# Kernel optimization log

Hardware: AMD Instinct MI355X
Metric: run time of the kernel (lower is better)

## Reference

```python
import jax, jax.numpy as jnp
import numpy as np

B, K, C, H, W = 8, 8, 128, 64, 64
RATE = 0.5
HW = H * W
NUM = int(RATE * HW)


def _l2norm(x, axis):
    # F.normalize: x / max(||x||, eps)
    n = jnp.linalg.norm(x, axis=axis, keepdims=True)
    return x / jnp.maximum(n, 1e-12)


def setup_inputs() -> dict:
    key = jax.random.key(0)
    k1, k2, k3 = jax.random.split(key, 3)
    feat = jax.random.normal(k1, (B, C, H, W), jnp.float32)
    refs = jax.random.normal(k2, (B, K, C, H, W), jnp.float32)
    sim = jax.random.uniform(k3, (B, K), jnp.float32)
    sim = sim / jnp.sum(sim, axis=1, keepdims=True)  # row-normalized as in Generator
    rng = np.random.default_rng(0)
    # random.sample -> unique spatial indices per batch row
    feat_indices = jnp.asarray(
        np.stack([rng.permutation(HW)[:NUM] for _ in range(B)]), jnp.int32)
    return {"feat": feat, "refs": refs, "similarity": sim,
            "feat_indices": feat_indices, "index": 0}


def reference(feat, refs, similarity, feat_indices, index):
    b, k, c, h, w = refs.shape
    hw = h * w
    n = k - 1
    # drop the base reference at `index`
    refs_ex = jnp.concatenate([refs[:, :index], refs[:, index + 1:]], axis=1)  # [b,n,c,h,w]
    base_sim = similarity[:, index]                                            # [b]
    ref_sims = jnp.concatenate([similarity[:, :index], similarity[:, index + 1:]], axis=1)  # [b,n]

    feat2 = feat.reshape(b, c, hw)                       # [b,c,hw]
    w_feat = _l2norm(jnp.swapaxes(feat2, 1, 2), 2)       # [b,hw,c], unit over c
    refs2 = refs_ex.reshape(b, n, c, hw)                 # [b,n,c,hw]
    w_refs = _l2norm(refs2, 2)                           # unit over c

    # gather the sampled query positions
    feat_select = jnp.take_along_axis(feat2, feat_indices[:, None, :], axis=2)   # [b,c,num]
    w_feat_sel = jnp.take_along_axis(w_feat, feat_indices[:, :, None], axis=1)   # [b,num,c]
    w_feat_sel = _l2norm(w_feat_sel, 2)

    def retrieve(args):
        w_ref, ref = args                                  # [b,c,hw] each
        fx = jnp.einsum('bqc,bch->bqh', w_feat_sel, w_ref)  # cosine scores [b,num,hw]
        idx = jnp.argmax(fx, axis=2)                        # top-1 -> [b,num]
        sel = jnp.take_along_axis(ref, idx[:, None, :], axis=2)  # [b,c,num]
        return idx, sel

    # sequential over n=k-1 refs (matches original loop, keeps peak memory at one
    # [b,num,hw] score matrix at a time)
    ref_idx, ref_sel = jax.lax.map(
        retrieve, (jnp.moveaxis(w_refs, 1, 0), jnp.moveaxis(refs2, 1, 0)))
    ref_indices = jnp.swapaxes(ref_idx, 0, 1)            # [b,n,num]
    ref_selects = jnp.moveaxis(ref_sel, 0, 1)            # [b,n,c,num]

    # similarity-weighted fusion
    fused = base_sim[:, None, None] * feat_select \
        + jnp.einsum('bn,bncq->bcq', ref_sims, ref_selects)   # [b,c,num]

    # batched scatter back into the feature map
    out = feat2.at[jnp.arange(b)[:, None, None],
                   jnp.arange(c)[None, :, None],
                   feat_indices[:, None, :]].set(fused)
    return out.reshape(b, c, h, w), feat_indices, ref_indices
```

## Files before the change

kernel.cpp:

```cpp
#include <hip/hip_runtime.h>
#include <math.h>

#define B_    8
#define K_    8
#define C_    128
#define HW_   4096
#define NUM_  2048
#define N_    7

#define WS_A_OFF    0
#define WS_SELQ_OFF (B_*NUM_*C_)
#define WS_KBUF_OFF (WS_SELQ_OFF + B_*K_*HW_)
#define WS_IDX_OFF  (WS_KBUF_OFF + B_*N_*NUM_*8)
#define WS_A2_OFF   (WS_IDX_OFF + B_*N_*NUM_)
#define WS_GHI_OFF  (WS_A2_OFF + B_*NUM_*C_)
#define GPLANE_V4   (B_*K_*16*HW_)

typedef __bf16 bf16x8 __attribute__((ext_vector_type(8)));
typedef float  f32x4  __attribute__((ext_vector_type(4)));
typedef unsigned int u32x4 __attribute__((ext_vector_type(4)));

static __device__ __forceinline__ f32x4 mf16(bf16x8 a, bf16x8 b, f32x4 c) {
    return __builtin_amdgcn_mfma_f32_16x16x32_bf16(a, b, c, 0, 0, 0);
}

static __device__ __forceinline__ unsigned bfhi16(float x) {
    unsigned b = __float_as_uint(x);
    return (b + 0x7fffu + ((b >> 16) & 1u)) >> 16;
}
static __device__ __forceinline__ void split2(float x, float y,
                                              unsigned &hp, unsigned &lp) {
    unsigned hx = bfhi16(x), hy = bfhi16(y);
    float rx = x - __uint_as_float(hx << 16);
    float ry = y - __uint_as_float(hy << 16);
    hp = hx | (hy << 16);
    lp = bfhi16(rx) | (bfhi16(ry) << 16);
}

static __device__ __forceinline__ float fmul_nc(float a, float b) {
    float r = a * b;
    asm volatile("" : "+v"(r));
    return r;
}
static __device__ __forceinline__ float fadd_nc(float a, float b) {
    float r = a + b;
    asm volatile("" : "+v"(r));
    return r;
}

static __device__ __forceinline__ void gll16(const u32x4* g, u32x4* l) {
    __builtin_amdgcn_global_load_lds(
        (const __attribute__((address_space(1))) void*)g,
        (__attribute__((address_space(3))) void*)l, 16, 0, 0);
}

__global__ void prep_split(const float* __restrict__ refs,
                           u32x4* __restrict__ Ghi,
                           u32x4* __restrict__ Glo) {
    __shared__ float part[8][32];
    __shared__ float ivs[32];
    int blk = blockIdx.x;
    int h0  = (blk & (HW_ / 32 - 1)) * 32;
    int bk  = blk >> 7;
    int t = threadIdx.x;
    int h = t & 31, oct = t >> 5;
    const float* p = refs + ((size_t)bk * C_ + oct * 16) * HW_ + h0 + h;
    float v[16];
    float ss = 0.f;
#pragma unroll
    for (int m = 0; m < 16; ++m) {
        v[m] = p[(size_t)m * HW_];
        ss = fmaf(v[m], v[m], ss);
    }
    part[oct][h] = ss;
    __syncthreads();
    if (t < 32) {
        float s = part[0][t];
#pragma unroll
        for (int o = 1; o < 8; ++o) s += part[o][t];
        ivs[t] = 1.0f / fmaxf(sqrtf(s), 1e-12f);
    }
    __syncthreads();
    float iv = ivs[h];
    u32x4 H0, L0, H1, L1;
#pragma unroll
    for (int m = 0; m < 4; ++m) {
        unsigned hp, lp;
        split2(v[2*m] * iv, v[2*m+1] * iv, hp, lp);
        H0[m] = hp; L0[m] = lp;
    }
#pragma unroll
    for (int m = 0; m < 4; ++m) {
        unsigned hp, lp;
        split2(v[8+2*m] * iv, v[9+2*m] * iv, hp, lp);
        H1[m] = hp; L1[m] = lp;
    }
    size_t o0 = (size_t)(bk * 16 + 2*oct)     * HW_ + h0 + h;
    size_t o1 = (size_t)(bk * 16 + 2*oct + 1) * HW_ + h0 + h;
    Ghi[o0] = H0; Glo[o0] = L0;
    Ghi[o1] = H1; Glo[o1] = L1;
}

__global__ void aprep2_kernel(const float* __restrict__ feat,
                              const int* __restrict__ fidx,
                              float* __restrict__ A,
                              float* __restrict__ A2,
                              int* __restrict__ selq,
                              float* __restrict__ out1) {
    int w    = (blockIdx.x * blockDim.x + threadIdx.x) >> 6;
    int lane = threadIdx.x & 63;
    int fi = fidx[w];
    int b  = w >> 11;
    const float* src = feat + (size_t)b * C_ * HW_ + fi;
    float v0 = src[(size_t)lane * HW_];
    float v1 = src[(size_t)(lane + 64) * HW_];
    float ss = fmaf(v0, v0, v1 * v1);
#pragma unroll
    for (int off = 32; off; off >>= 1) ss += __shfl_xor(ss, off);
    float rn = 1.0f / fmaxf(sqrtf(ss), 1e-12f);
    size_t o = (size_t)w * C_;
    A[o + lane]       = v0;
    A[o + lane + 64]  = v1;
    A2[o + lane]      = v0 * rn;
    A2[o + lane + 64] = v1 * rn;
    if (lane == 0) {
        selq[b * HW_ + fi] = w & (NUM_ - 1);
        out1[w] = (float)fi;
    }
}

__global__ __launch_bounds__(256, 4) void gemm_gll_topk2(
        const float* __restrict__ A2,
        const u32x4* __restrict__ Ghi, const u32x4* __restrict__ Glo,
        const int* __restrict__ pindex,
        uint4* __restrict__ kbuf) {
    __shared__ u32x4 Bsh[2][2][512];

    const int tid = threadIdx.x;
    const int l = tid & 63, wq = tid >> 6;
    const int ll = l & 15, lh = l >> 4;

    int bid = blockIdx.x;
    int swz = (bid & 7) * 224 + (bid >> 3);
    int pair = swz >> 5;
    int rem  = swz & 31;
    int qt = rem >> 1, hs = rem & 1;
    int b = pair / N_, n = pair % N_;
    int index = pindex[0];
    int ks = n + (n >= index ? 1 : 0);
    const int hbase0 = hs * 2048;

    const float* Ap = A2 + ((size_t)b * NUM_ + qt * 128 + wq * 32) * C_;
    const u32x4* Gh = Ghi + (size_t)(b * K_ + ks) * 16 * HW_ + hbase0;
    const u32x4* Gl = Glo + (size_t)(b * K_ + ks) * 16 * HW_ + hbase0;

    bf16x8 ahi[2][4], alo[2][4];
#pragma unroll
    for (int mf = 0; mf < 2; ++mf)
#pragma unroll
        for (int kk = 0; kk < 4; ++kk) {
            const float* ap = Ap + (mf * 16 + ll) * C_ + kk * 32 + lh * 8;
            float4 xa = *(const float4*)ap;
            float4 xb = *(const float4*)(ap + 4);
            float xs[8] = {xa.x, xa.y, xa.z, xa.w, xb.x, xb.y, xb.z, xb.w};
            u32x4 H, L;
#pragma unroll
            for (int p = 0; p < 4; ++p) {
                unsigned hp, lp;
                split2(xs[2*p], xs[2*p+1], hp, lp);
                H[p] = hp; L[p] = lp;
            }
            ahi[mf][kk] = __builtin_bit_cast(bf16x8, H);
            alo[mf][kk] = __builtin_bit_cast(bf16x8, L);
        }

    unsigned k1[8], k2[8];
#pragma unroll
    for (int rw = 0; rw < 8; ++rw) { k1[rw] = 0u; k2[rw] = 0u; }

    const int lin0 = tid, lin1 = 256 + tid;
    const size_t go0 = (size_t)(lin0 >> 5) * HW_ + (lin0 & 31);
    const size_t go1 = (size_t)(lin1 >> 5) * HW_ + (lin1 & 31);

#define STAGE(buf, htv) do {                                   \
        gll16(Gh + go0 + (htv), &Bsh[buf][0][lin0]);           \
        gll16(Gh + go1 + (htv), &Bsh[buf][0][lin1]);           \
        gll16(Gl + go0 + (htv), &Bsh[buf][1][lin0]);           \
        gll16(Gl + go1 + (htv), &Bsh[buf][1][lin1]);           \
    } while (0)

    STAGE(0, 0);
    __syncthreads();

    for (int t = 0; t < 64; ++t) {
        const int cur = t & 1;
        const int ht = t * 32;

        if (t < 63) STAGE(cur ^ 1, ht + 32);

        f32x4 acc[2][2];
#pragma unroll
        for (int mf = 0; mf < 2; ++mf)
#pragma unroll
            for (int nf = 0; nf < 2; ++nf) acc[mf][nf] = 6.0f;

#pragma unroll
        for (int kk = 0; kk < 4; ++kk) {
#pragma unroll
            for (int nf = 0; nf < 2; ++nf) {
                int off = (kk * 4 + lh) * 32 + nf * 16 + ll;
                bf16x8 bh = __builtin_bit_cast(bf16x8, Bsh[cur][0][off]);
                bf16x8 bl = __builtin_bit_cast(bf16x8, Bsh[cur][1][off]);
#pragma unroll
                for (int mf = 0; mf < 2; ++mf) {
                    f32x4 a_ = acc[mf][nf];
                    a_ = mf16(ahi[mf][kk], bh, a_);
                    a_ = mf16(ahi[mf][kk], bl, a_);
                    a_ = mf16(alo[mf][kk], bh, a_);
                    acc[mf][nf] = a_;
                }
            }
        }

#pragma unroll
        for (int nf = 0; nf < 2; ++nf) {
            unsigned hv = (unsigned)(hbase0 + ht + nf * 16 + ll);
#pragma unroll
            for (int mf = 0; mf < 2; ++mf)
#pragma unroll
                for (int r = 0; r < 4; ++r) {
                    int rw = mf * 4 + r;
                    unsigned u = __float_as_uint(acc[mf][nf][r]);
                    unsigned key = ((u & 0x007FFFF8u) << 9) | hv;
                    unsigned mn = min(k1[rw], key);
                    k1[rw] = max(k1[rw], key);
                    k2[rw] = max(k2[rw], mn);
                }
        }

        __syncthreads();
    }
#undef STAGE

#define CEU(X,Y) { if (mv[Y] > mv[X]) { unsigned t_ = mv[X]; mv[X] = mv[Y]; mv[Y] = t_; } }
#pragma unroll
    for (int rw = 0; rw < 8; ++rw) {
        unsigned av[4] = {k1[rw], k2[rw], 0u, 0u};
#pragma unroll
        for (int s = 1; s <= 8; s <<= 1) {
            unsigned bv[4];
#pragma unroll
            for (int j = 0; j < 4; ++j)
                bv[j] = (unsigned)__shfl_xor((int)av[j], s);
            unsigned mv[4];
#pragma unroll
            for (int j = 0; j < 4; ++j)
                mv[j] = (av[j] > bv[3-j]) ? av[j] : bv[3-j];
            CEU(0, 2) CEU(1, 3) CEU(0, 1) CEU(2, 3)
#pragma unroll
            for (int j = 0; j < 4; ++j) av[j] = mv[j];
        }
        if (ll == 0) {
            int q = qt * 128 + wq * 32 + (rw >> 2) * 16 + lh * 4 + (rw & 3);
            size_t o = ((size_t)(b * N_ + n) * NUM_ + q) * 2 + hs;
            kbuf[o] = make_uint4(av[0], av[1], av[2], av[3]);
        }
    }
#undef CEU
}

static __device__ float pairwise128_sumsq_div(const float* __restrict__ x,
                                              float d) {
    float r[8];
#pragma unroll
    for (int j = 0; j < 8; ++j) {
        float v = __fdiv_rn(x[j], d);
        r[j] = fmul_nc(v, v);
    }
    for (int i = 8; i < C_; i += 8) {
#pragma unroll
        for (int j = 0; j < 8; ++j) {
            float v = __fdiv_rn(x[i + j], d);
            r[j] = fadd_nc(r[j], fmul_nc(v, v));
        }
    }
    return fadd_nc(fadd_nc(fadd_nc(r[0], r[1]), fadd_nc(r[2], r[3])),
                   fadd_nc(fadd_nc(r[4], r[5]), fadd_nc(r[6], r[7])));
}

static __device__ float emul_score_batched(const float* __restrict__ w2a,
                                           const float* __restrict__ Rb,
                                           int h) {
    float rv[C_];
#pragma unroll
    for (int c = 0; c < C_; ++c) rv[c] = Rb[(size_t)c * HW_ + h];
    float sr = fmul_nc(rv[0], rv[0]);
#pragma unroll
    for (int c = 1; c < C_; ++c)
        sr = fadd_nc(sr, fmul_nc(rv[c], rv[c]));
    float nr = fmaxf(__fsqrt_rn(sr), 1e-12f);
    float acc = 0.f;
#pragma unroll
    for (int c = 0; c < C_; ++c) {
        float wr = __fdiv_rn(rv[c], nr);
        acc = fadd_nc(acc, fmul_nc(w2a[c], wr));
    }
    return acc;
}

__global__ __launch_bounds__(256, 1) void rescore_emul8(
        const float* __restrict__ A,
        const float* __restrict__ refs,
        const int* __restrict__ pindex,
        const uint4* __restrict__ kbuf,
        float thr,
        int* __restrict__ idxout,
        float* __restrict__ out2) {
    int r = blockIdx.x * blockDim.x + threadIdx.x;
    if (r >= B_ * N_ * NUM_) return;
    uint4 ka = kbuf[(size_t)r * 2 + 0];
    uint4 kb = kbuf[(size_t)r * 2 + 1];
    unsigned kk[8] = {ka.x, ka.y, ka.z, ka.w, kb.x, kb.y, kb.z, kb.w};
    unsigned s1 = 0u, s2 = 0u;
#pragma unroll
    for (int j = 0; j < 8; ++j) {
        unsigned mn = min(s1, kk[j]);
        s1 = max(s1, kk[j]);
        s2 = max(s2, mn);
    }
    int win;
    unsigned top = s1 >> 12;
    if ((float)(top - (s2 >> 12)) > thr) {
        win = (int)(s1 & 0xFFFu);
    } else {
        int q  = r & (NUM_ - 1);
        int bn = r >> 11;
        int b = bn / N_, n = bn % N_;
        int index = pindex[0];
        int ks = n + (n >= index ? 1 : 0);
        const float* qp = A    + ((size_t)b * NUM_ + q) * C_;
        const float* Rb = refs + (size_t)(b * K_ + ks) * C_ * HW_;
        float s1f = pairwise128_sumsq_div(qp, 1.0f);
        float n1 = fmaxf(__fsqrt_rn(s1f), 1e-12f);
        float s2f = pairwise128_sumsq_div(qp, n1);
        float n2 = fmaxf(__fsqrt_rn(s2f), 1e-12f);
        float w2a[C_];
#pragma unroll
        for (int c = 0; c < C_; ++c)
            w2a[c] = __fdiv_rn(__fdiv_rn(qp[c], n1), n2);
        win = -1; float bw = -INFINITY;
        for (int j = 0; j < 8; ++j) {
            if ((float)(top - (kk[j] >> 12)) > thr) continue;
            int h = (int)(kk[j] & 0xFFFu);
            float s = emul_score_batched(w2a, Rb, h);
            if (s > bw || (s == bw && h < win)) { bw = s; win = h; }
        }
    }
    idxout[r] = win;
    out2[r]   = (float)win;
}

__global__ void fused_copy_scatter(const float* __restrict__ feat,
                                   const float* __restrict__ refs,
                                   const float* __restrict__ sim,
                                   const int* __restrict__ selq,
                                   const int* __restrict__ pindex,
                                   const int* __restrict__ idxf,
                                   float* __restrict__ out0) {
    int i = blockIdx.x * blockDim.x + threadIdx.x;
    int h4 = (i & (HW_ / 4 - 1)) << 2;
    int c  = (i >> 10) & (C_ - 1);
    int b  = i >> 17;
    size_t off = ((size_t)b * C_ + c) * HW_ + h4;
    f32x4 v = *(const f32x4*)(feat + off);
    int4 q4 = *(const int4*)(selq + b * HW_ + h4);
    int qs[4] = {q4.x, q4.y, q4.z, q4.w};
    if (qs[0] >= 0 || qs[1] >= 0 || qs[2] >= 0 || qs[3] >= 0) {
        int index = pindex[0];
        float bs = sim[b * K_ + index];
        const float* rbase = refs + (size_t)b * K_ * C_ * HW_ + (size_t)c * HW_;
#pragma unroll
        for (int j = 0; j < 4; ++j) {
            if (qs[j] < 0) continue;
            float acc = bs * v[j];
#pragma unroll
            for (int n = 0; n < N_; ++n) {
                int ks = n + (n >= index ? 1 : 0);
                int id = idxf[(size_t)(b * N_ + n) * NUM_ + qs[j]];
                acc = fmaf(sim[b * K_ + ks],
                           rbase[(size_t)ks * C_ * HW_ + id], acc);
            }
            v[j] = acc;
        }
    }
    *(f32x4*)(out0 + off) = v;
}

extern "C" void kernel_launch(void* const* d_in, const int* in_sizes, int n_in,
                              void* d_out, int out_size, void* d_ws, size_t ws_size,
                              hipStream_t stream) {
    const float* feat = (const float*)d_in[0];
    const float* refs = (const float*)d_in[1];
    const float* sim  = (const float*)d_in[2];
    const int*   fidx = (const int*)d_in[3];
    const int*   pidx = (const int*)d_in[4];

    float* wsf   = (float*)d_ws;
    float* A     = wsf + WS_A_OFF;
    int*   selq  = (int*)(wsf + WS_SELQ_OFF);
    uint4* kbuf  = (uint4*)(wsf + WS_KBUF_OFF);
    int*   idxf  = (int*)(wsf + WS_IDX_OFF);
    float* A2    = wsf + WS_A2_OFF;
    u32x4* Ghi   = (u32x4*)(wsf + WS_GHI_OFF);
    u32x4* Glo   = Ghi + GPLANE_V4;

    float* out0 = (float*)d_out;
    float* out1 = out0 + (size_t)B_ * C_ * HW_;
    float* out2 = out1 + (size_t)B_ * NUM_;

    hipMemsetAsync(selq, 0xFF, (size_t)B_ * HW_ * sizeof(int), stream);
    prep_split<<<B_ * K_ * (HW_ / 32), 256, 0, stream>>>(refs, Ghi, Glo);
    aprep2_kernel<<<(B_ * NUM_) / 4, 256, 0, stream>>>(feat, fidx, A, A2,
                                                       selq, out1);
    gemm_gll_topk2<<<56 * 16 * 2, 256, 0, stream>>>(A2, Ghi, Glo, pidx, kbuf);
    rescore_emul8<<<(B_ * N_ * NUM_ + 255) / 256, 256, 0, stream>>>(
        A, refs, pidx, kbuf, 8.5f, idxf, out2);
    fused_copy_scatter<<<(B_ * C_ * HW_ / 4) / 256, 256, 0, stream>>>(
        feat, refs, sim, selq, pidx, idxf, out0);
}
```

Measured before the change: 531.1 us.

## Switch top-k GEMM to 32x32x16 MFMA tiles with med3-based top-2 update

Result: slower. 572.6 us (+7.8%).

```diff
diff --git a/kernel.cpp b/kernel.cpp
--- a/kernel.cpp
+++ b/kernel.cpp
@@ -18,10 +18,11 @@
 
 typedef __bf16 bf16x8 __attribute__((ext_vector_type(8)));
 typedef float  f32x4  __attribute__((ext_vector_type(4)));
+typedef float  f32x16 __attribute__((ext_vector_type(16)));
 typedef unsigned int u32x4 __attribute__((ext_vector_type(4)));
 
-static __device__ __forceinline__ f32x4 mf16(bf16x8 a, bf16x8 b, f32x4 c) {
-    return __builtin_amdgcn_mfma_f32_16x16x32_bf16(a, b, c, 0, 0, 0);
+static __device__ __forceinline__ f32x16 mf32(bf16x8 a, bf16x8 b, f32x16 c) {
+    return __builtin_amdgcn_mfma_f32_32x32x16_bf16(a, b, c, 0, 0, 0);
 }
 
 static __device__ __forceinline__ unsigned bfhi16(float x) {
@@ -129,7 +130,7 @@
     }
 }
 
-__global__ __launch_bounds__(256, 4) void gemm_gll_topk2(
+__global__ __launch_bounds__(256, 3) void gemm_gll_topk3(
         const float* __restrict__ A2,
         const u32x4* __restrict__ Ghi, const u32x4* __restrict__ Glo,
         const int* __restrict__ pindex,
@@ -138,7 +139,7 @@
 
     const int tid = threadIdx.x;
     const int l = tid & 63, wq = tid >> 6;
-    const int ll = l & 15, lh = l >> 4;
+    const int l31 = l & 31, lhf = l >> 5;
 
     int bid = blockIdx.x;
     int swz = (bid & 7) * 224 + (bid >> 3);
@@ -154,29 +155,27 @@
     const u32x4* Gh = Ghi + (size_t)(b * K_ + ks) * 16 * HW_ + hbase0;
     const u32x4* Gl = Glo + (size_t)(b * K_ + ks) * 16 * HW_ + hbase0;
 
-    bf16x8 ahi[2][4], alo[2][4];
-#pragma unroll
-    for (int mf = 0; mf < 2; ++mf)
-#pragma unroll
-        for (int kk = 0; kk < 4; ++kk) {
-            const float* ap = Ap + (mf * 16 + ll) * C_ + kk * 32 + lh * 8;
-            float4 xa = *(const float4*)ap;
-            float4 xb = *(const float4*)(ap + 4);
-            float xs[8] = {xa.x, xa.y, xa.z, xa.w, xb.x, xb.y, xb.z, xb.w};
-            u32x4 H, L;
-#pragma unroll
-            for (int p = 0; p < 4; ++p) {
-                unsigned hp, lp;
-                split2(xs[2*p], xs[2*p+1], hp, lp);
-                H[p] = hp; L[p] = lp;
-            }
-            ahi[mf][kk] = __builtin_bit_cast(bf16x8, H);
-            alo[mf][kk] = __builtin_bit_cast(bf16x8, L);
-        }
-
-    unsigned k1[8], k2[8];
-#pragma unroll
-    for (int rw = 0; rw < 8; ++rw) { k1[rw] = 0u; k2[rw] = 0u; }
+    bf16x8 ahi[8], alo[8];
+#pragma unroll
+    for (int kk = 0; kk < 8; ++kk) {
+        const float* ap = Ap + l31 * C_ + kk * 16 + lhf * 8;
+        float4 xa = *(const float4*)ap;
+        float4 xb = *(const float4*)(ap + 4);
+        float xs[8] = {xa.x, xa.y, xa.z, xa.w, xb.x, xb.y, xb.z, xb.w};
+        u32x4 H, L;
+#pragma unroll
+        for (int p = 0; p < 4; ++p) {
+            unsigned hp, lp;
+            split2(xs[2*p], xs[2*p+1], hp, lp);
+            H[p] = hp; L[p] = lp;
+        }
+        ahi[kk] = __builtin_bit_cast(bf16x8, H);
+        alo[kk] = __builtin_bit_cast(bf16x8, L);
+    }
+
+    unsigned k1[16], k2[16];
+#pragma unroll
+    for (int rw = 0; rw < 16; ++rw) { k1[rw] = 0u; k2[rw] = 0u; }
 
     const int lin0 = tid, lin1 = 256 + tid;
     const size_t go0 = (size_t)(lin0 >> 5) * HW_ + (lin0 & 31);
@@ -192,51 +191,36 @@
     STAGE(0, 0);
     __syncthreads();
 
+    unsigned hvt = (unsigned)(hbase0 + l31);
+
     for (int t = 0; t < 64; ++t) {
         const int cur = t & 1;
         const int ht = t * 32;
 
         if (t < 63) STAGE(cur ^ 1, ht + 32);
 
-        f32x4 acc[2][2];
-#pragma unroll
-        for (int mf = 0; mf < 2; ++mf)
-#pragma unroll
-            for (int nf = 0; nf < 2; ++nf) acc[mf][nf] = 6.0f;
-
-#pragma unroll
-        for (int kk = 0; kk < 4; ++kk) {
-#pragma unroll
-            for (int nf = 0; nf < 2; ++nf) {
-                int off = (kk * 4 + lh) * 32 + nf * 16 + ll;
-                bf16x8 bh = __builtin_bit_cast(bf16x8, Bsh[cur][0][off]);
-                bf16x8 bl = __builtin_bit_cast(bf16x8, Bsh[cur][1][off]);
-#pragma unroll
-                for (int mf = 0; mf < 2; ++mf) {
-                    f32x4 a_ = acc[mf][nf];
-                    a_ = mf16(ahi[mf][kk], bh, a_);
-                    a_ = mf16(ahi[mf][kk], bl, a_);
-                    a_ = mf16(alo[mf][kk], bh, a_);
-                    acc[mf][nf] = a_;
-                }
-            }
-        }
-
-#pragma unroll
-        for (int nf = 0; nf < 2; ++nf) {
-            unsigned hv = (unsigned)(hbase0 + ht + nf * 16 + ll);
-#pragma unroll
-            for (int mf = 0; mf < 2; ++mf)
-#pragma unroll
-                for (int r = 0; r < 4; ++r) {
-                    int rw = mf * 4 + r;
-                    unsigned u = __float_as_uint(acc[mf][nf][r]);
-                    unsigned key = ((u & 0x007FFFF8u) << 9) | hv;
-                    unsigned mn = min(k1[rw], key);
-                    k1[rw] = max(k1[rw], key);
-                    k2[rw] = max(k2[rw], mn);
-                }
-        }
+        f32x16 acc = 6.0f;
+#pragma unroll
+        for (int kk = 0; kk < 8; ++kk) {
+            int off = (kk * 2 + lhf) * 32 + l31;
+            bf16x8 bh = __builtin_bit_cast(bf16x8, Bsh[cur][0][off]);
+            bf16x8 bl = __builtin_bit_cast(bf16x8, Bsh[cur][1][off]);
+            acc = mf32(ahi[kk], bh, acc);
+            acc = mf32(ahi[kk], bl, acc);
+            acc = mf32(alo[kk], bh, acc);
+        }
+
+#pragma unroll
+        for (int rw = 0; rw < 16; ++rw) {
+            unsigned u = __float_as_uint(acc[rw]);
+            unsigned key = ((u << 9) & 0xFFFFF000u) | hvt;
+            unsigned nk2;
+            asm("v_med3_u32 %0, %1, %2, %3"
+                : "=v"(nk2) : "v"(k1[rw]), "v"(k2[rw]), "v"(key));
+            k2[rw] = nk2;
+            k1[rw] = max(k1[rw], key);
+        }
+        hvt += 32;
 
         __syncthreads();
     }
@@ -244,10 +228,10 @@
 
 #define CEU(X,Y) { if (mv[Y] > mv[X]) { unsigned t_ = mv[X]; mv[X] = mv[Y]; mv[Y] = t_; } }
 #pragma unroll
-    for (int rw = 0; rw < 8; ++rw) {
+    for (int rw = 0; rw < 16; ++rw) {
         unsigned av[4] = {k1[rw], k2[rw], 0u, 0u};
 #pragma unroll
-        for (int s = 1; s <= 8; s <<= 1) {
+        for (int s = 1; s <= 16; s <<= 1) {
             unsigned bv[4];
 #pragma unroll
             for (int j = 0; j < 4; ++j)
@@ -260,8 +244,9 @@
 #pragma unroll
             for (int j = 0; j < 4; ++j) av[j] = mv[j];
         }
-        if (ll == 0) {
-            int q = qt * 128 + wq * 32 + (rw >> 2) * 16 + lh * 4 + (rw & 3);
+        if (l31 == 0) {
+            int row = (rw & 3) + 8 * (rw >> 2) + 4 * lhf;
+            int q = qt * 128 + wq * 32 + row;
             size_t o = ((size_t)(b * N_ + n) * NUM_ + q) * 2 + hs;
             kbuf[o] = make_uint4(av[0], av[1], av[2], av[3]);
         }
@@ -422,7 +407,7 @@
     prep_split<<<B_ * K_ * (HW_ / 32), 256, 0, stream>>>(refs, Ghi, Glo);
     aprep2_kernel<<<(B_ * NUM_) / 4, 256, 0, stream>>>(feat, fidx, A, A2,
                                                        selq, out1);
-    gemm_gll_topk2<<<56 * 16 * 2, 256, 0, stream>>>(A2, Ghi, Glo, pidx, kbuf);
+    gemm_gll_topk3<<<56 * 16 * 2, 256, 0, stream>>>(A2, Ghi, Glo, pidx, kbuf);
     rescore_emul8<<<(B_ * N_ * NUM_ + 255) / 256, 256, 0, stream>>>(
         A, refs, pidx, kbuf, 8.5f, idxf, out2);
     fused_copy_scatter<<<(B_ * C_ * HW_ / 4) / 256, 256, 0, stream>>>(
```
